# Kernel tuning notes

Hardware: AMD Instinct MI355X
Metric: run time of the kernel (lower is better)

The kernel has to match this reference:

```python
import jax, jax.numpy as jnp
import numpy as np

N, F_IN, R, H, U, B, E = 20000, 256, 8, 4, 64, 4, 320000
NEG_SLOPE = 0.2  # torch F.leaky_relu default is 0.01, but GAT/RGAT uses 0.2; source uses F.leaky_relu -> 0.01
LRELU_SLOPE = 0.01


def setup_inputs() -> dict:
    key = jax.random.key(0)
    ks = jax.random.split(key, 8)
    x = jax.random.normal(ks[0], (N, F_IN), dtype=jnp.float32)
    basis = jax.random.normal(ks[1], (B, F_IN, U), dtype=jnp.float32) * 0.05
    coeff = jax.random.normal(ks[2], (R * H, B), dtype=jnp.float32)
    attn_q = jax.random.normal(ks[3], (R, H, U), dtype=jnp.float32) * 0.1
    attn_k = jax.random.normal(ks[4], (R, H, U), dtype=jnp.float32) * 0.1
    src = jax.random.randint(ks[5], (E,), 0, N, dtype=jnp.int32)
    dst = jax.random.randint(ks[6], (E,), 0, N, dtype=jnp.int32)
    rel = jax.random.randint(ks[7], (E,), 0, R, dtype=jnp.int32)
    return {"x": x, "basis": basis, "coeff": coeff, "attn_q": attn_q,
            "attn_k": attn_k, "src": src, "dst": dst, "rel": rel}


def reference(x, basis, coeff, attn_q, attn_k, src, dst, rel):
    n = x.shape[0]
    # Basis-decomposed relational kernels: W_{r,h} = sum_b c_{(r,h),b} W'_b
    W = jnp.einsum("cb,bfu->cfu", coeff, basis).reshape(R, H, F_IN, U)
    # Relation/head-specific projections: [N, R, H, U]
    xp = jnp.einsum("nf,rhfu->nrhu", x, W)
    # GAT-style 'sum' attention, attention_units=1: scalar query/key per (node, r, h)
    q = jnp.einsum("nrhu,rhu->nrh", xp, attn_q)  # [N, R, H]
    k = jnp.einsum("nrhu,rhu->nrh", xp, attn_k)  # [N, R, H]
    # Per-edge logits, gathered along sparse support: [E, H]
    logit = jax.nn.leaky_relu(q[src, rel] + k[dst, rel], negative_slope=LRELU_SLOPE)
    # ARGAT: segment softmax per destination node across all relations/edges
    m = jax.ops.segment_max(logit, dst, num_segments=n)        # [N, H]
    m = jnp.where(jnp.isfinite(m), m, 0.0)
    ex = jnp.exp(logit - m[dst])                               # [E, H]
    denom = jax.ops.segment_sum(ex, dst, num_segments=n)       # [N, H]
    alpha = ex / jnp.maximum(denom[dst], 1e-16)                # [E, H]
    # Weighted scatter-aggregation of messages: [N, H, U]
    msg = xp[src, rel] * alpha[:, :, None]                     # [E, H, U]
    out = jax.ops.segment_sum(msg, dst, num_segments=n)
    # head_aggregation='mean', activation=None, use_bias=False
    return out.mean(axis=1)  # [N, U]
```

## Files before the change

### kernel.cpp

```cpp
#include <hip/hip_runtime.h>
#include <hip/hip_bf16.h>
#include <math.h>

#define F_IN    256
#define R_REL   8
#define H_HEADS 4
#define U_DIM   64
#define B_BASES 4
#define C_TOT   (R_REL * H_HEADS)
#define LRELU   0.01f
#define SLOT_CAP 64

typedef __attribute__((ext_vector_type(8))) short short8;
typedef __attribute__((ext_vector_type(4))) float f32x4;

__device__ __forceinline__ unsigned short f2bf(float f) {
    unsigned int u = __float_as_uint(f);
    u = (u + 0x7FFF + ((u >> 16) & 1)) >> 16;
    return (unsigned short)u;
}
__device__ __forceinline__ float bf2f_lo(unsigned int v) { return __uint_as_float(v << 16); }
__device__ __forceinline__ float bf2f_hi(unsigned int v) { return __uint_as_float(v & 0xFFFF0000u); }

__global__ __launch_bounds__(256) void prep_all(const float* __restrict__ x,
                                                unsigned short* __restrict__ xb,
                                                int total4,
                                                int* __restrict__ counts,
                                                int n_nodes,
                                                const float* __restrict__ basis,
                                                const float* __restrict__ coeff,
                                                const float* __restrict__ attn_q,
                                                const float* __restrict__ attn_k,
                                                unsigned short* __restrict__ Wt,
                                                int n_cast_blocks) {
    if (blockIdx.x < (unsigned)n_cast_blocks) {
        int i = blockIdx.x * 256 + threadIdx.x;
        if (i < n_nodes) counts[i] = 0;
        if (i >= total4) return;
        float4 v = *(const float4*)&x[(size_t)i * 4];
        ushort4 o;
        o.x = f2bf(v.x); o.y = f2bf(v.y); o.z = f2bf(v.z); o.w = f2bf(v.w);
        *(ushort4*)&xb[(size_t)i * 4] = o;
        return;
    }

    __shared__ float aq[64], ak[64];
    int c = blockIdx.x - n_cast_blocks;
    int f = threadIdx.x;
    if (f < 64) {
        aq[f] = attn_q[c * 64 + f];
        ak[f] = attn_k[c * 64 + f];
    }
    __syncthreads();

    #pragma unroll
    for (int j = 0; j < 8; ++j) {
        int nn = c * 8 + j;
        int b = nn & 3, u = nn >> 2;
        Wt[(size_t)nn * 256 + f] = f2bf(basis[(size_t)b * (F_IN * U_DIM) + (size_t)f * U_DIM + u]);
    }

    float sq = 0.f, sk = 0.f;
    #pragma unroll
    for (int b = 0; b < B_BASES; ++b) {
        float cb = coeff[c * 4 + b];
        const float* bp = basis + (size_t)b * (F_IN * U_DIM) + (size_t)f * U_DIM;
        float dq = 0.f, dk = 0.f;
        #pragma unroll
        for (int u = 0; u < 64; ++u) {
            float v = bp[u];
            dq += v * aq[u];
            dk += v * ak[u];
        }
        sq += cb * dq;
        sk += cb * dk;
    }
    Wt[(size_t)(256 + c) * 256 + f] = f2bf(sq);
    Wt[(size_t)(288 + c) * 256 + f] = f2bf(sk);
}

__global__ __launch_bounds__(256) void gemm_scatter(const unsigned short* __restrict__ xb,
                                                    const unsigned short* __restrict__ Wt,
                                                    unsigned short* __restrict__ zb,
                                                    float* __restrict__ qk,
                                                    const int* __restrict__ src,
                                                    const int* __restrict__ dst,
                                                    const int* __restrict__ rel,
                                                    int* __restrict__ counts,
                                                    unsigned int* __restrict__ slots,
                                                    int nrows, int E) {
    if (blockIdx.y == 5) {
        int stride = gridDim.x * 256;
        int base = blockIdx.x * 256 + threadIdx.x;
        #pragma unroll
        for (int j = 0; j < 8; ++j) {
            int i = base + j * stride;
            if (i < E) {
                int d = dst[i];
                int pos = atomicAdd(&counts[d], 1);
                if (pos < SLOT_CAP)
                    slots[(size_t)d * SLOT_CAP + pos] = (unsigned)src[i] | ((unsigned)rel[i] << 20);
            }
        }
        return;
    }

    __shared__ unsigned short Al[128 * 72];
    __shared__ unsigned short Bl[64 * 72];

    const int tid  = threadIdx.x;
    const int wave = tid >> 6;
    const int lane = tid & 63;
    const int wr   = wave >> 1;
    const int wc   = wave & 1;
    const int m0   = blockIdx.x * 128;
    const int bb   = blockIdx.y;
    const int l15  = lane & 15;
    const int quad = lane >> 4;

    f32x4 acc[4][2];
    #pragma unroll
    for (int t = 0; t < 4; ++t)
        #pragma unroll
        for (int s = 0; s < 2; ++s)
            acc[t][s] = (f32x4){0.f, 0.f, 0.f, 0.f};

    for (int k0 = 0; k0 < 256; k0 += 64) {
        #pragma unroll
        for (int p = 0; p < 4; ++p) {
            int idx = p * 256 + tid;
            int row = idx >> 3;
            int cg  = idx & 7;
            int gr  = m0 + row;
            uint4 v = make_uint4(0, 0, 0, 0);
            if (gr < nrows) v = *(const uint4*)&xb[(size_t)gr * 256 + k0 + cg * 8];
            *(uint4*)&Al[row * 72 + cg * 8] = v;
        }
        #pragma unroll
        for (int p = 0; p < 2; ++p) {
            int idx = p * 256 + tid;
            int row = idx >> 3;
            int cg  = idx & 7;
            uint4 v = *(const uint4*)&Wt[(size_t)(bb * 64 + row) * 256 + k0 + cg * 8];
            *(uint4*)&Bl[row * 72 + cg * 8] = v;
        }
        __syncthreads();

        #pragma unroll
        for (int ks = 0; ks < 64; ks += 32) {
            short8 bfr[2];
            #pragma unroll
            for (int s = 0; s < 2; ++s)
                bfr[s] = *(short8*)&Bl[(wc * 32 + s * 16 + l15) * 72 + ks + quad * 8];
            #pragma unroll
            for (int t = 0; t < 4; ++t) {
                short8 afr = *(short8*)&Al[(wr * 64 + t * 16 + l15) * 72 + ks + quad * 8];
                #pragma unroll
                for (int s = 0; s < 2; ++s)
                    acc[t][s] = __builtin_amdgcn_mfma_f32_16x16x32_bf16(afr, bfr[s], acc[t][s], 0, 0, 0);
            }
        }
        __syncthreads();
    }

    #pragma unroll
    for (int t = 0; t < 4; ++t) {
        #pragma unroll
        for (int s = 0; s < 2; ++s) {
            int c_local = wc * 32 + s * 16 + l15;
            #pragma unroll
            for (int reg = 0; reg < 4; ++reg) {
                int m = m0 + wr * 64 + t * 16 + quad * 4 + reg;
                if (m < nrows) {
                    float v = acc[t][s][reg];
                    if (bb < 4) zb[(size_t)m * 256 + bb * 64 + c_local] = f2bf(v);
                    else        qk[(size_t)m * 64 + c_local] = v;
                }
            }
        }
    }
}

__global__ __launch_bounds__(256) void agg_kernel(const unsigned short* __restrict__ zb,
                                                  const float* __restrict__ qk,
                                                  const float* __restrict__ coeff,
                                                  const unsigned int* __restrict__ slots,
                                                  const int* __restrict__ counts,
                                                  float* __restrict__ out,
                                                  int n_nodes) {
    __shared__ float cf[128];
    __shared__ float4 gsh[4][64];
    __shared__ int    ssh[4][64];
    if (threadIdx.x < 128) cf[threadIdx.x] = coeff[threadIdx.x];
    __syncthreads();

    int wv   = threadIdx.x >> 6;
    int n    = blockIdx.x * 4 + wv;
    int lane = threadIdx.x & 63;
    if (n >= n_nodes) return;

    int cnt = counts[n];
    if (cnt > SLOT_CAP) cnt = SLOT_CAP;
    const unsigned int* sl = slots + (size_t)n * SLOT_CAP;

    float e0 = 0.f, e1 = 0.f, e2 = 0.f, e3 = 0.f;
    int s_edge = 0, r_edge = 0;
    if (lane < cnt) {
        unsigned p = sl[lane];
        s_edge = (int)(p & 0xFFFFFu);
        r_edge = (int)(p >> 20);
        float4 q  = *(const float4*)&qk[(size_t)s_edge * 64 + r_edge * 4];
        float4 kv = *(const float4*)&qk[(size_t)n * 64 + 32 + r_edge * 4];
        float l0 = q.x + kv.x, l1 = q.y + kv.y, l2 = q.z + kv.z, l3 = q.w + kv.w;
        l0 = (l0 > 0.f) ? l0 : LRELU * l0;
        l1 = (l1 > 0.f) ? l1 : LRELU * l1;
        l2 = (l2 > 0.f) ? l2 : LRELU * l2;
        l3 = (l3 > 0.f) ? l3 : LRELU * l3;
        e0 = __expf(l0); e1 = __expf(l1); e2 = __expf(l2); e3 = __expf(l3);
    }
    float d0 = e0, d1 = e1, d2 = e2, d3 = e3;
    #pragma unroll
    for (int off = 32; off; off >>= 1) {
        d0 += __shfl_xor(d0, off);
        d1 += __shfl_xor(d1, off);
        d2 += __shfl_xor(d2, off);
        d3 += __shfl_xor(d3, off);
    }
    if (lane < cnt) {
        float a0 = e0 * ((d0 > 0.f) ? 0.25f / d0 : 0.f);
        float a1 = e1 * ((d1 > 0.f) ? 0.25f / d1 : 0.f);
        float a2 = e2 * ((d2 > 0.f) ? 0.25f / d2 : 0.f);
        float a3 = e3 * ((d3 > 0.f) ? 0.25f / d3 : 0.f);
        const float* c0 = &cf[(r_edge * 4 + 0) * 4];
        const float* c1 = &cf[(r_edge * 4 + 1) * 4];
        const float* c2 = &cf[(r_edge * 4 + 2) * 4];
        const float* c3 = &cf[(r_edge * 4 + 3) * 4];
        float4 g4;
        g4.x = a0 * c0[0] + a1 * c1[0] + a2 * c2[0] + a3 * c3[0];
        g4.y = a0 * c0[1] + a1 * c1[1] + a2 * c2[1] + a3 * c3[1];
        g4.z = a0 * c0[2] + a1 * c1[2] + a2 * c2[2] + a3 * c3[2];
        g4.w = a0 * c0[3] + a1 * c1[3] + a2 * c2[3] + a3 * c3[3];
        gsh[wv][lane] = g4;
        ssh[wv][lane] = s_edge;
    }

    int es = lane >> 3;
    int g  = lane & 7;
    float acc[4][2];
    #pragma unroll
    for (int v = 0; v < 4; ++v) { acc[v][0] = 0.f; acc[v][1] = 0.f; }

    for (int base = 0; base < cnt; base += 8) {
        int i = base + es;
        if (i < cnt) {
            float4 g4 = gsh[wv][i];
            int s = ssh[wv][i];
            const unsigned short* zr = zb + (size_t)s * 256 + g * 8;
            #pragma unroll
            for (int v = 0; v < 4; ++v) {
                uint4 z4 = *(const uint4*)(zr + v * 64);
                acc[v][0] += g4.x * bf2f_lo(z4.x) + g4.y * bf2f_hi(z4.x) +
                             g4.z * bf2f_lo(z4.y) + g4.w * bf2f_hi(z4.y);
                acc[v][1] += g4.x * bf2f_lo(z4.z) + g4.y * bf2f_hi(z4.z) +
                             g4.z * bf2f_lo(z4.w) + g4.w * bf2f_hi(z4.w);
            }
        }
    }

    #pragma unroll
    for (int v = 0; v < 4; ++v) {
        #pragma unroll
        for (int j = 0; j < 2; ++j) {
            acc[v][j] += __shfl_xor(acc[v][j], 8);
            acc[v][j] += __shfl_xor(acc[v][j], 16);
            acc[v][j] += __shfl_xor(acc[v][j], 32);
        }
    }
    if (es == 0) {
        #pragma unroll
        for (int v = 0; v < 4; ++v) {
            float2 o = make_float2(acc[v][0], acc[v][1]);
            *(float2*)&out[(size_t)n * 64 + v * 16 + g * 2] = o;
        }
    }
}

extern "C" void kernel_launch(void* const* d_in, const int* in_sizes, int n_in,
                              void* d_out, int out_size, void* d_ws, size_t ws_size,
                              hipStream_t stream) {
    const float* x      = (const float*)d_in[0];
    const float* basis  = (const float*)d_in[1];
    const float* coeff  = (const float*)d_in[2];
    const float* attn_q = (const float*)d_in[3];
    const float* attn_k = (const float*)d_in[4];
    const int*   src    = (const int*)d_in[5];
    const int*   dst    = (const int*)d_in[6];
    const int*   rel    = (const int*)d_in[7];
    float* out = (float*)d_out;

    const int n_nodes = in_sizes[0] / F_IN;
    const int E       = in_sizes[5];

    char* ws = (char*)d_ws;
    size_t off = 0;
    auto alloc = [&](size_t bytes) -> void* {
        void* p = ws + off;
        off += bytes;
        off = (off + 255) & ~(size_t)255;
        return p;
    };
    unsigned short* xb   = (unsigned short*)alloc((size_t)n_nodes * 256 * 2);
    unsigned short* Wt   = (unsigned short*)alloc((size_t)320 * 256 * 2);
    unsigned short* zb   = (unsigned short*)alloc((size_t)n_nodes * 256 * 2);
    float* qk            = (float*)alloc((size_t)n_nodes * 64 * 4);
    unsigned int* slots  = (unsigned int*)alloc((size_t)n_nodes * SLOT_CAP * 4);
    int* counts          = (int*)alloc((size_t)n_nodes * 4);

    const int total4 = n_nodes * 64;
    const int n_cast_blocks = (total4 + 255) / 256;

    prep_all<<<n_cast_blocks + C_TOT, 256, 0, stream>>>(
        x, xb, total4, counts, n_nodes, basis, coeff, attn_q, attn_k, Wt, n_cast_blocks);

    dim3 g2((n_nodes + 127) / 128, 6);
    gemm_scatter<<<g2, 256, 0, stream>>>(xb, Wt, zb, qk, src, dst, rel, counts, slots,
                                         n_nodes, E);

    agg_kernel<<<(n_nodes + 3) / 4, 256, 0, stream>>>(zb, qk, coeff, slots, counts, out, n_nodes);
}
```

Baseline: 139.5 us.

## Fuse x bf16 cast into GEMM and compute all 320 output columns per block

Removes the separate fp32→bf16 cast pass and its intermediate buffer: the GEMM now reads fp32 x directly and converts while staging into shared memory. Each block handles 64 rows against all 320 weight columns, so x is read once instead of five times across column blocks. The edge-scatter work moves to 32 extra blocks with a strided loop. The trade-off is more LDS per block (about 55KB), 80 accumulator registers per thread, and restaging the full weight tile for every row block, which may lower occupancy.

```diff
diff --git a/kernel.cpp b/kernel.cpp
--- a/kernel.cpp
+++ b/kernel.cpp
@@ -22,30 +22,19 @@
 __device__ __forceinline__ float bf2f_lo(unsigned int v) { return __uint_as_float(v << 16); }
 __device__ __forceinline__ float bf2f_hi(unsigned int v) { return __uint_as_float(v & 0xFFFF0000u); }
 
-__global__ __launch_bounds__(256) void prep_all(const float* __restrict__ x,
-                                                unsigned short* __restrict__ xb,
-                                                int total4,
-                                                int* __restrict__ counts,
-                                                int n_nodes,
-                                                const float* __restrict__ basis,
+__global__ __launch_bounds__(256) void prep_all(const float* __restrict__ basis,
                                                 const float* __restrict__ coeff,
                                                 const float* __restrict__ attn_q,
                                                 const float* __restrict__ attn_k,
                                                 unsigned short* __restrict__ Wt,
-                                                int n_cast_blocks) {
-    if (blockIdx.x < (unsigned)n_cast_blocks) {
-        int i = blockIdx.x * 256 + threadIdx.x;
-        if (i < n_nodes) counts[i] = 0;
-        if (i >= total4) return;
-        float4 v = *(const float4*)&x[(size_t)i * 4];
-        ushort4 o;
-        o.x = f2bf(v.x); o.y = f2bf(v.y); o.z = f2bf(v.z); o.w = f2bf(v.w);
-        *(ushort4*)&xb[(size_t)i * 4] = o;
-        return;
-    }
+                                                int* __restrict__ counts,
+                                                int n_nodes) {
+    int i = blockIdx.x * 256 + threadIdx.x;
+    if (i < n_nodes) counts[i] = 0;
+    if (blockIdx.x >= C_TOT) return;
 
     __shared__ float aq[64], ak[64];
-    int c = blockIdx.x - n_cast_blocks;
+    int c = blockIdx.x;
     int f = threadIdx.x;
     if (f < 64) {
         aq[f] = attn_q[c * 64 + f];
@@ -79,102 +68,99 @@
     Wt[(size_t)(288 + c) * 256 + f] = f2bf(sk);
 }
 
-__global__ __launch_bounds__(256) void gemm_scatter(const unsigned short* __restrict__ xb,
-                                                    const unsigned short* __restrict__ Wt,
-                                                    unsigned short* __restrict__ zb,
-                                                    float* __restrict__ qk,
-                                                    const int* __restrict__ src,
-                                                    const int* __restrict__ dst,
-                                                    const int* __restrict__ rel,
-                                                    int* __restrict__ counts,
-                                                    unsigned int* __restrict__ slots,
-                                                    int nrows, int E) {
-    if (blockIdx.y == 5) {
-        int stride = gridDim.x * 256;
-        int base = blockIdx.x * 256 + threadIdx.x;
-        #pragma unroll
-        for (int j = 0; j < 8; ++j) {
-            int i = base + j * stride;
-            if (i < E) {
-                int d = dst[i];
-                int pos = atomicAdd(&counts[d], 1);
-                if (pos < SLOT_CAP)
-                    slots[(size_t)d * SLOT_CAP + pos] = (unsigned)src[i] | ((unsigned)rel[i] << 20);
-            }
+__global__ __launch_bounds__(256) void gemm_all(const float* __restrict__ x,
+                                                const unsigned short* __restrict__ Wt,
+                                                unsigned short* __restrict__ zb,
+                                                float* __restrict__ qk,
+                                                const int* __restrict__ src,
+                                                const int* __restrict__ dst,
+                                                const int* __restrict__ rel,
+                                                int* __restrict__ counts,
+                                                unsigned int* __restrict__ slots,
+                                                int nrows, int E, int n_m_blocks) {
+    if ((int)blockIdx.x >= n_m_blocks) {
+        int sb = blockIdx.x - n_m_blocks;
+        int stride = 32 * 256;
+        for (int i = sb * 256 + threadIdx.x; i < E; i += stride) {
+            int d = dst[i];
+            int pos = atomicAdd(&counts[d], 1);
+            if (pos < SLOT_CAP)
+                slots[(size_t)d * SLOT_CAP + pos] = (unsigned)src[i] | ((unsigned)rel[i] << 20);
         }
         return;
     }
 
-    __shared__ unsigned short Al[128 * 72];
-    __shared__ unsigned short Bl[64 * 72];
+    __shared__ unsigned short Al[64 * 72];
+    __shared__ unsigned short Bl[320 * 72];
 
     const int tid  = threadIdx.x;
     const int wave = tid >> 6;
     const int lane = tid & 63;
     const int wr   = wave >> 1;
     const int wc   = wave & 1;
-    const int m0   = blockIdx.x * 128;
-    const int bb   = blockIdx.y;
+    const int m0   = blockIdx.x * 64;
     const int l15  = lane & 15;
     const int quad = lane >> 4;
 
-    f32x4 acc[4][2];
-    #pragma unroll
-    for (int t = 0; t < 4; ++t)
-        #pragma unroll
-        for (int s = 0; s < 2; ++s)
+    f32x4 acc[2][10];
+    #pragma unroll
+    for (int t = 0; t < 2; ++t)
+        #pragma unroll
+        for (int s = 0; s < 10; ++s)
             acc[t][s] = (f32x4){0.f, 0.f, 0.f, 0.f};
 
     for (int k0 = 0; k0 < 256; k0 += 64) {
         #pragma unroll
         for (int p = 0; p < 4; ++p) {
+            int idx = p * 256 + tid;
+            int row = idx >> 4;
+            int cg  = idx & 15;
+            int gr  = m0 + row;
+            float4 v = make_float4(0.f, 0.f, 0.f, 0.f);
+            if (gr < nrows) v = *(const float4*)&x[(size_t)gr * 256 + k0 + cg * 4];
+            ushort4 o;
+            o.x = f2bf(v.x); o.y = f2bf(v.y); o.z = f2bf(v.z); o.w = f2bf(v.w);
+            *(ushort4*)&Al[row * 72 + cg * 4] = o;
+        }
+        #pragma unroll
+        for (int p = 0; p < 10; ++p) {
             int idx = p * 256 + tid;
             int row = idx >> 3;
             int cg  = idx & 7;
-            int gr  = m0 + row;
-            uint4 v = make_uint4(0, 0, 0, 0);
-            if (gr < nrows) v = *(const uint4*)&xb[(size_t)gr * 256 + k0 + cg * 8];
-            *(uint4*)&Al[row * 72 + cg * 8] = v;
-        }
-        #pragma unroll
-        for (int p = 0; p < 2; ++p) {
-            int idx = p * 256 + tid;
-            int row = idx >> 3;
-            int cg  = idx & 7;
-            uint4 v = *(const uint4*)&Wt[(size_t)(bb * 64 + row) * 256 + k0 + cg * 8];
+            uint4 v = *(const uint4*)&Wt[(size_t)row * 256 + k0 + cg * 8];
             *(uint4*)&Bl[row * 72 + cg * 8] = v;
         }
         __syncthreads();
 
         #pragma unroll
         for (int ks = 0; ks < 64; ks += 32) {
-            short8 bfr[2];
+            short8 afr[2];
             #pragma unroll
-            for (int s = 0; s < 2; ++s)
-                bfr[s] = *(short8*)&Bl[(wc * 32 + s * 16 + l15) * 72 + ks + quad * 8];
+            for (int t = 0; t < 2; ++t)
+                afr[t] = *(short8*)&Al[(wr * 32 + t * 16 + l15) * 72 + ks + quad * 8];
             #pragma unroll
-            for (int t = 0; t < 4; ++t) {
-                short8 afr = *(short8*)&Al[(wr * 64 + t * 16 + l15) * 72 + ks + quad * 8];
+            for (int s = 0; s < 10; ++s) {
+                short8 bfr = *(short8*)&Bl[(wc * 160 + s * 16 + l15) * 72 + ks + quad * 8];
                 #pragma unroll
-                for (int s = 0; s < 2; ++s)
-                    acc[t][s] = __builtin_amdgcn_mfma_f32_16x16x32_bf16(afr, bfr[s], acc[t][s], 0, 0, 0);
+                for (int t = 0; t < 2; ++t)
+                    acc[t][s] = __builtin_amdgcn_mfma_f32_16x16x32_bf16(afr[t], bfr, acc[t][s], 0, 0, 0);
             }
         }
         __syncthreads();
     }
 
     #pragma unroll
-    for (int t = 0; t < 4; ++t) {
-        #pragma unroll
-        for (int s = 0; s < 2; ++s) {
-            int c_local = wc * 32 + s * 16 + l15;
+    for (int t = 0; t < 2; ++t) {
+        #pragma unroll
+        for (int s = 0; s < 10; ++s) {
+            int n = wc * 160 + s * 16 + l15;
             #pragma unroll
             for (int reg = 0; reg < 4; ++reg) {
-                int m = m0 + wr * 64 + t * 16 + quad * 4 + reg;
+                int m = m0 + wr * 32 + t * 16 + quad * 4 + reg;
                 if (m < nrows) {
                     float v = acc[t][s][reg];
-                    if (bb < 4) zb[(size_t)m * 256 + bb * 64 + c_local] = f2bf(v);
-                    else        qk[(size_t)m * 64 + c_local] = v;
+                    if (n < 256) zb[(size_t)m * 256 + n] = f2bf(v);
+                    else         qk[(size_t)m * 64 + (n - 256)] = v;
                 }
             }
         }
@@ -309,22 +295,19 @@
         off = (off + 255) & ~(size_t)255;
         return p;
     };
-    unsigned short* xb   = (unsigned short*)alloc((size_t)n_nodes * 256 * 2);
     unsigned short* Wt   = (unsigned short*)alloc((size_t)320 * 256 * 2);
     unsigned short* zb   = (unsigned short*)alloc((size_t)n_nodes * 256 * 2);
     float* qk            = (float*)alloc((size_t)n_nodes * 64 * 4);
     unsigned int* slots  = (unsigned int*)alloc((size_t)n_nodes * SLOT_CAP * 4);
     int* counts          = (int*)alloc((size_t)n_nodes * 4);
 
-    const int total4 = n_nodes * 64;
-    const int n_cast_blocks = (total4 + 255) / 256;
-
-    prep_all<<<n_cast_blocks + C_TOT, 256, 0, stream>>>(
-        x, xb, total4, counts, n_nodes, basis, coeff, attn_q, attn_k, Wt, n_cast_blocks);
-
-    dim3 g2((n_nodes + 127) / 128, 6);
-    gemm_scatter<<<g2, 256, 0, stream>>>(xb, Wt, zb, qk, src, dst, rel, counts, slots,
-                                         n_nodes, E);
+    int n_prep_blocks = (n_nodes + 255) / 256;
+    prep_all<<<n_prep_blocks, 256, 0, stream>>>(basis, coeff, attn_q, attn_k, Wt,
+                                                counts, n_nodes);
+
+    int n_m_blocks = (n_nodes + 63) / 64;
+    gemm_all<<<n_m_blocks + 32, 256, 0, stream>>>(x, Wt, zb, qk, src, dst, rel,
+                                                  counts, slots, n_nodes, E, n_m_blocks);
 
     agg_kernel<<<(n_nodes + 3) / 4, 256, 0, stream>>>(zb, qk, coeff, slots, counts, out, n_nodes);
 }
```

Measured after the change: 162.1 us. 1.16x slower.
